# Kernel tuning notes

Measured on AMD Instinct MI355X. Metric: run time of the kernel, lower is better.

Reference implementation:

```python
import jax, jax.numpy as jnp
import numpy as np

B, V, D = 1024, 50000, 300
EPS = 1e-7


def setup_inputs() -> dict:
    key = jax.random.key(0)
    k1, k2 = jax.random.split(key)
    # soft multi-hot label mask over the vocab (torch code multiplies floats)
    labels = jax.random.uniform(k1, (B, V), dtype=jnp.float32)
    # pretrained word2vec-style embedding table
    weight = jax.random.normal(k2, (V, D), dtype=jnp.float32)
    return {"labels": labels, "weight": weight}


def reference(labels, weight):
    # torch: mul(weight, labels[:, :, None]).sum(1)  ==  labels @ weight
    attr = jnp.einsum('bv,vd->bd', labels, weight)  # (B, D)
    # L2 normalize: attr / (sqrt(sum(attr^2, 1)) + 1e-7)
    norm = jnp.sqrt(jnp.sum(attr * attr, axis=1, keepdims=True))
    return attr / (norm + EPS)
```

## Files before the change

### kernel.cpp

```cpp
#include <hip/hip_runtime.h>
#include <hip/hip_bf16.h>
#include <math.h>

typedef __bf16 bf16;
typedef bf16 bf16x8 __attribute__((ext_vector_type(8)));
typedef float f32x4 __attribute__((ext_vector_type(4)));

constexpr int Mdim = 1024;
constexpr int Kdim = 50000;
constexpr int Ndim = 300;
constexpr int NP   = 320;

constexpr int BM = 64, BN = 320, BK = 64;
constexpr int MT = Mdim / BM;
constexpr int ROWB = BK * 2;

__device__ __forceinline__ bf16x8 bzero8() {
    bf16x8 v;
#pragma unroll
    for (int e = 0; e < 8; ++e) v[e] = (bf16)0.0f;
    return v;
}

__device__ __forceinline__ bf16* swz(bf16* base, int row, int colByte) {
    return (bf16*)((char*)base + row * ROWB + (colByte ^ ((row & 7) << 4)));
}
__device__ __forceinline__ const bf16* swz(const bf16* base, int row, int colByte) {
    return (const bf16*)((const char*)base + row * ROWB + (colByte ^ ((row & 7) << 4)));
}

constexpr int TK = 64;
constexpr int TS = 301;
__global__ __launch_bounds__(256) void transpose_w(const float* __restrict__ W,
                                                   bf16* __restrict__ Wt)
{
    __shared__ bf16 tile[TK * TS];
    const int k0 = blockIdx.x * TK;
    const int t  = threadIdx.x;

    for (int c = t; c < 64 * 75; c += 256) {
        const int kk = c / 75;
        const int ch = c % 75;
        const int k  = k0 + kk;
        float4 v = make_float4(0.f, 0.f, 0.f, 0.f);
        if (k < Kdim) v = *(const float4*)(W + (size_t)k * Ndim + ch * 4);
        bf16* p = &tile[kk * TS + ch * 4];
        p[0] = (bf16)v.x; p[1] = (bf16)v.y; p[2] = (bf16)v.z; p[3] = (bf16)v.w;
    }
    __syncthreads();
    for (int c = t; c < NP * 8; c += 256) {
        const int n  = c >> 3;
        const int ch = c & 7;
        const int k  = k0 + ch * 8;
        if (k + 8 <= Kdim) {
            bf16x8 v = bzero8();
            if (n < Ndim) {
#pragma unroll
                for (int j = 0; j < 8; ++j) v[j] = tile[(ch * 8 + j) * TS + n];
            }
            *(bf16x8*)(Wt + (size_t)n * Kdim + k) = v;
        }
    }
}

template<int SPLIT, int SEGLEN, bool ATOMIC>
__global__ __launch_bounds__(512, 4) void gemm_kernel(const float* __restrict__ A,
                                                      const bf16* __restrict__ Wt,
                                                      float* __restrict__ out)
{
    __shared__ bf16 As[BM * BK];
    __shared__ bf16 Bs[BN * BK];

    const int bx   = blockIdx.x;
    const int mt   = bx & (MT - 1);
    const int ks   = bx >> 4;
    const int m0   = mt * BM;
    const int kbeg = ks * SEGLEN;
    const int kend = min(kbeg + SEGLEN, Kdim);

    const int t    = threadIdx.x;
    const int lane = t & 63;
    const int wave = t >> 6;
    const int wm   = wave >> 2;
    const int wn   = wave & 3;
    const int lm   = lane & 15;
    const int lq   = lane >> 4;

    const int arow = t >> 3;
    const int acol = (t & 7) * 8;
    const float* aptr = A + (size_t)(m0 + arow) * Kdim;

    float4 af[2];
    bf16x8 bfr[5];

    auto load_tiles = [&](int k0) {
        const int k = k0 + acol;
        if (k + 8 <= kend) {
            af[0] = *(const float4*)(aptr + k);
            af[1] = *(const float4*)(aptr + k + 4);
        } else {
            af[0] = make_float4(0.f, 0.f, 0.f, 0.f);
            af[1] = make_float4(0.f, 0.f, 0.f, 0.f);
        }
#pragma unroll
        for (int i = 0; i < 5; ++i) {
            const int c = t + 512 * i;
            const int brow = c >> 3;
            const int bcol = (c & 7) * 8;
            const int kk = k0 + bcol;
            bfr[i] = (kk + 8 <= kend) ? *(const bf16x8*)(Wt + (size_t)brow * Kdim + kk)
                                      : bzero8();
        }
    };
    auto store_tiles = [&]() {
        bf16x8 v;
        v[0]=(bf16)af[0].x; v[1]=(bf16)af[0].y; v[2]=(bf16)af[0].z; v[3]=(bf16)af[0].w;
        v[4]=(bf16)af[1].x; v[5]=(bf16)af[1].y; v[6]=(bf16)af[1].z; v[7]=(bf16)af[1].w;
        *(bf16x8*)swz(As, arow, acol * 2) = v;
#pragma unroll
        for (int i = 0; i < 5; ++i) {
            const int c = t + 512 * i;
            const int brow = c >> 3;
            const int bcol = (c & 7) * 8;
            *(bf16x8*)swz(Bs, brow, bcol * 2) = bfr[i];
        }
    };

    f32x4 acc[2][5] = {};

    load_tiles(kbeg);
    for (int k0 = kbeg; k0 < kend; k0 += BK) {
        store_tiles();
        __syncthreads();
        if (k0 + BK < kend) load_tiles(k0 + BK);
#pragma unroll
        for (int s = 0; s < 2; ++s) {
            bf16x8 a[2], b[5];
#pragma unroll
            for (int i = 0; i < 2; ++i)
                a[i] = *(const bf16x8*)swz(As, wm * 32 + i * 16 + lm, s * 64 + lq * 16);
#pragma unroll
            for (int j = 0; j < 5; ++j)
                b[j] = *(const bf16x8*)swz(Bs, wn * 80 + j * 16 + lm, s * 64 + lq * 16);
#pragma unroll
            for (int i = 0; i < 2; ++i)
#pragma unroll
                for (int j = 0; j < 5; ++j)
                    acc[i][j] = __builtin_amdgcn_mfma_f32_16x16x32_bf16(a[i], b[j], acc[i][j], 0, 0, 0);
        }
        __syncthreads();
    }

    const int col0 = wn * 80 + lm;
    const int rloc = wm * 32 + lq * 4;
    if (ATOMIC) {
#pragma unroll
        for (int i = 0; i < 2; ++i)
#pragma unroll
            for (int j = 0; j < 5; ++j)
#pragma unroll
                for (int r = 0; r < 4; ++r)
                    atomicAdd(&out[(size_t)(m0 + rloc + i * 16 + r) * NP + col0 + j * 16],
                              acc[i][j][r]);
    } else {
        float* P = out + (size_t)ks * Mdim * NP;
#pragma unroll
        for (int i = 0; i < 2; ++i)
#pragma unroll
            for (int j = 0; j < 5; ++j)
#pragma unroll
                for (int r = 0; r < 4; ++r)
                    P[(size_t)(m0 + rloc + i * 16 + r) * NP + col0 + j * 16] = acc[i][j][r];
    }
}

__global__ __launch_bounds__(320) void reduce_norm_k(const float* __restrict__ P,
                                                     float* __restrict__ out,
                                                     int split)
{
    const int b = blockIdx.x;
    const int t = threadIdx.x;
    float v = 0.f;
    for (int ks = 0; ks < split; ++ks)
        v += P[((size_t)ks * Mdim + b) * NP + t];
    float ss = v * v;
#pragma unroll
    for (int o = 32; o > 0; o >>= 1) ss += __shfl_down(ss, o, 64);
    __shared__ float wsum[5];
    __shared__ float scale;
    if ((t & 63) == 0) wsum[t >> 6] = ss;
    __syncthreads();
    if (t == 0) {
        float s = wsum[0] + wsum[1] + wsum[2] + wsum[3] + wsum[4];
        scale = 1.0f / (sqrtf(s) + 1e-7f);
    }
    __syncthreads();
    if (t < Ndim) out[(size_t)b * Ndim + t] = v * scale;
}

__global__ __launch_bounds__(320) void normalize_k(const float* __restrict__ Cacc,
                                                   float* __restrict__ out)
{
    const int b = blockIdx.x;
    const int t = threadIdx.x;
    float v = 0.f;
    if (t < Ndim) v = Cacc[(size_t)b * NP + t];
    float ss = v * v;
#pragma unroll
    for (int o = 32; o > 0; o >>= 1) ss += __shfl_down(ss, o, 64);
    __shared__ float wsum[5];
    __shared__ float scale;
    if ((t & 63) == 0) wsum[t >> 6] = ss;
    __syncthreads();
    if (t == 0) {
        float s = wsum[0] + wsum[1] + wsum[2] + wsum[3] + wsum[4];
        scale = 1.0f / (sqrtf(s) + 1e-7f);
    }
    __syncthreads();
    if (t < Ndim) out[(size_t)b * Ndim + t] = v * scale;
}

extern "C" void kernel_launch(void* const* d_in, const int* in_sizes, int n_in,
                              void* d_out, int out_size, void* d_ws, size_t ws_size,
                              hipStream_t stream)
{
    const float* labels = (const float*)d_in[0];
    const float* weight = (const float*)d_in[1];
    float* out = (float*)d_out;

    bf16* Wt = (bf16*)d_ws;
    const size_t wtBytes  = (size_t)NP * Kdim * sizeof(bf16);
    float* aux = (float*)((char*)d_ws + wtBytes);
    const size_t perSplit = (size_t)Mdim * NP * sizeof(float);

    transpose_w<<<dim3((Kdim + TK - 1) / TK), dim3(256), 0, stream>>>(weight, Wt);

    if (ws_size >= wtBytes + 49 * perSplit) {
        gemm_kernel<49, 1024, false><<<dim3(MT * 49), dim3(512), 0, stream>>>(labels, Wt, aux);
        reduce_norm_k<<<dim3(Mdim), dim3(320), 0, stream>>>(aux, out, 49);
    } else if (ws_size >= wtBytes + 16 * perSplit) {
        gemm_kernel<16, 3136, false><<<dim3(MT * 16), dim3(512), 0, stream>>>(labels, Wt, aux);
        reduce_norm_k<<<dim3(Mdim), dim3(320), 0, stream>>>(aux, out, 16);
    } else {
        hipMemsetAsync(aux, 0, perSplit, stream);
        gemm_kernel<49, 1024, true><<<dim3(MT * 49), dim3(512), 0, stream>>>(labels, Wt, aux);
        normalize_k<<<dim3(Mdim), dim3(320), 0, stream>>>(aux, out);
    }
}
```

Baseline: 401.7 us.

## Stage weight tiles via direct global-to-LDS loads with zero-padded K

Pads the transposed bf16 weight to a K stride of 50048 with zeros so the B tile needs no bounds checks. The B operand is then copied straight from global memory into shared memory with global_load_lds, with the XOR swizzle folded into the source address, instead of going through registers. The loop's sync placement changes: B is staged into LDS directly at the top of each iteration with no register prefetch, so its load latency may be exposed. In exchange it saves VGPRs and the store instructions.

```diff
diff --git a/kernel.cpp b/kernel.cpp
--- a/kernel.cpp
+++ b/kernel.cpp
@@ -8,6 +8,7 @@
 
 constexpr int Mdim = 1024;
 constexpr int Kdim = 50000;
+constexpr int Kpad = 50048;
 constexpr int Ndim = 300;
 constexpr int NP   = 320;
 
@@ -27,6 +28,12 @@
 }
 __device__ __forceinline__ const bf16* swz(const bf16* base, int row, int colByte) {
     return (const bf16*)((const char*)base + row * ROWB + (colByte ^ ((row & 7) << 4)));
+}
+
+__device__ __forceinline__ void dma16(const void* g, void* l) {
+    __builtin_amdgcn_global_load_lds(
+        (const __attribute__((address_space(1))) unsigned int*)g,
+        (__attribute__((address_space(3))) unsigned int*)l, 16, 0, 0);
 }
 
 constexpr int TK = 64;
@@ -52,14 +59,13 @@
         const int n  = c >> 3;
         const int ch = c & 7;
         const int k  = k0 + ch * 8;
-        if (k + 8 <= Kdim) {
-            bf16x8 v = bzero8();
-            if (n < Ndim) {
-#pragma unroll
-                for (int j = 0; j < 8; ++j) v[j] = tile[(ch * 8 + j) * TS + n];
-            }
-            *(bf16x8*)(Wt + (size_t)n * Kdim + k) = v;
-        }
+        bf16x8 v = bzero8();
+        if (n < Ndim) {
+#pragma unroll
+            for (int j = 0; j < 8; ++j)
+                v[j] = tile[(ch * 8 + j) * TS + n];
+        }
+        *(bf16x8*)(Wt + (size_t)n * Kpad + k) = v;
     }
 }
 
@@ -89,11 +95,9 @@
     const int arow = t >> 3;
     const int acol = (t & 7) * 8;
     const float* aptr = A + (size_t)(m0 + arow) * Kdim;
-
     float4 af[2];
-    bf16x8 bfr[5];
-
-    auto load_tiles = [&](int k0) {
+
+    auto loadA = [&](int k0) {
         const int k = k0 + acol;
         if (k + 8 <= kend) {
             af[0] = *(const float4*)(aptr + k);
@@ -102,37 +106,35 @@
             af[0] = make_float4(0.f, 0.f, 0.f, 0.f);
             af[1] = make_float4(0.f, 0.f, 0.f, 0.f);
         }
-#pragma unroll
-        for (int i = 0; i < 5; ++i) {
-            const int c = t + 512 * i;
-            const int brow = c >> 3;
-            const int bcol = (c & 7) * 8;
-            const int kk = k0 + bcol;
-            bfr[i] = (kk + 8 <= kend) ? *(const bf16x8*)(Wt + (size_t)brow * Kdim + kk)
-                                      : bzero8();
-        }
     };
-    auto store_tiles = [&]() {
+    auto storeA = [&]() {
         bf16x8 v;
         v[0]=(bf16)af[0].x; v[1]=(bf16)af[0].y; v[2]=(bf16)af[0].z; v[3]=(bf16)af[0].w;
         v[4]=(bf16)af[1].x; v[5]=(bf16)af[1].y; v[6]=(bf16)af[1].z; v[7]=(bf16)af[1].w;
         *(bf16x8*)swz(As, arow, acol * 2) = v;
+    };
+
+    const int r8   = lane >> 3;
+    const int cswz = ((lane & 7) ^ r8) * 16;
+    auto stageB = [&](int k0) {
 #pragma unroll
         for (int i = 0; i < 5; ++i) {
-            const int c = t + 512 * i;
-            const int brow = c >> 3;
-            const int bcol = (c & 7) * 8;
-            *(bf16x8*)swz(Bs, brow, bcol * 2) = bfr[i];
+            const int chunk = wave * 5 + i;
+            const int row   = chunk * 8 + r8;
+            const char* g = (const char*)Wt + ((size_t)row * Kpad + k0) * 2 + cswz;
+            dma16(g, (char*)Bs + chunk * 1024);
         }
     };
 
     f32x4 acc[2][5] = {};
 
-    load_tiles(kbeg);
+    loadA(kbeg);
     for (int k0 = kbeg; k0 < kend; k0 += BK) {
-        store_tiles();
         __syncthreads();
-        if (k0 + BK < kend) load_tiles(k0 + BK);
+        stageB(k0);
+        storeA();
+        if (k0 + BK < kend) loadA(k0 + BK);
+        __syncthreads();
 #pragma unroll
         for (int s = 0; s < 2; ++s) {
             bf16x8 a[2], b[5];
@@ -148,7 +150,6 @@
                 for (int j = 0; j < 5; ++j)
                     acc[i][j] = __builtin_amdgcn_mfma_f32_16x16x32_bf16(a[i], b[j], acc[i][j], 0, 0, 0);
         }
-        __syncthreads();
     }
 
     const int col0 = wn * 80 + lm;
@@ -229,11 +230,11 @@
     float* out = (float*)d_out;
 
     bf16* Wt = (bf16*)d_ws;
-    const size_t wtBytes  = (size_t)NP * Kdim * sizeof(bf16);
+    const size_t wtBytes  = (size_t)NP * Kpad * sizeof(bf16);
     float* aux = (float*)((char*)d_ws + wtBytes);
     const size_t perSplit = (size_t)Mdim * NP * sizeof(float);
 
-    transpose_w<<<dim3((Kdim + TK - 1) / TK), dim3(256), 0, stream>>>(weight, Wt);
+    transpose_w<<<dim3(Kpad / TK), dim3(256), 0, stream>>>(weight, Wt);
 
     if (ws_size >= wtBytes + 49 * perSplit) {
         gemm_kernel<49, 1024, false><<<dim3(MT * 49), dim3(512), 0, stream>>>(labels, Wt, aux);
```

Result: faster. 378.1 us (-5.9%).
